# Optimization experiments

Hardware: AMD Instinct MI355X
Metric: run time of the kernel (lower is better)

## Reference

```python
import jax, jax.numpy as jnp
import numpy as np

N_HEADS = 8
D_EMBED = 512
D_HEAD = D_EMBED // N_HEADS  # used only for the scale factor, as in the source


def setup_inputs() -> dict:
    key = jax.random.key(0)
    k1, k2, k3, k4, k5 = jax.random.split(key, 5)
    B, S, D = 4, 4096, D_EMBED
    s = 1.0 / np.sqrt(D)
    return {
        "x": jax.random.normal(k1, (B, S, D), dtype=jnp.float32),
        "w_in": jax.random.normal(k2, (3 * D, D), dtype=jnp.float32) * s,
        "b_in": jax.random.normal(k3, (3 * D,), dtype=jnp.float32) * 0.01,
        "w_out": jax.random.normal(k4, (D, D), dtype=jnp.float32) * s,
        "b_out": jax.random.normal(k5, (D,), dtype=jnp.float32) * 0.01,
    }


def reference(x, w_in, b_in, w_out, b_out):
    # in_proj: torch Linear y = x @ W.T + b ; chunk into q,k,v along last dim
    qkv = jnp.einsum("bsd,ed->bse", x, w_in) + b_in  # [B,S,3D]
    q, k, v = jnp.split(qkv, 3, axis=-1)  # each [B,S,D]
    # NOTE: source never splits into heads; attention over full d_embed,
    # but scaled by sqrt(d_head) = sqrt(d_embed / n_heads).
    scores = jnp.einsum("bqd,bkd->bqk", q, k) / np.sqrt(D_HEAD)  # [B,S,S]
    weight = jax.nn.softmax(scores, axis=-1)
    out = jnp.einsum("bqk,bkd->bqd", weight, v)  # [B,S,D]
    out = jnp.einsum("bsd,ed->bse", out, w_out) + b_out
    return out
```

## Files before the change

### kernel.cpp

```cpp
#include <hip/hip_runtime.h>

typedef __bf16 bf16x8 __attribute__((ext_vector_type(8)));
typedef float f32x4 __attribute__((ext_vector_type(4)));

#define MFMA16(a, b, c) __builtin_amdgcn_mfma_f32_16x16x32_bf16(a, b, c, 0, 0, 0)
#define LOG2E 1.44269504088896340736f

__device__ __forceinline__ unsigned short f2bf(float f) {
  union { float f; unsigned u; } v; v.f = f;
  return (unsigned short)((v.u + 0x7fffu + ((v.u >> 16) & 1u)) >> 16);
}
__device__ __forceinline__ bf16x8 ld_frag(const unsigned short* p) {
  return *(const bf16x8*)p;
}
__device__ __forceinline__ void gld_lds16(const unsigned short* g, unsigned short* l) {
  __builtin_amdgcn_global_load_lds(
      (const __attribute__((address_space(1))) unsigned int*)(const void*)g,
      (__attribute__((address_space(3))) unsigned int*)(void*)l, 16, 0, 0);
}

__global__ void cvt_f2bf(const float* __restrict__ in,
                         unsigned short* __restrict__ out, int n4) {
  int i = blockIdx.x * blockDim.x + threadIdx.x;
  if (i < n4) {
    float4 v = ((const float4*)in)[i];
    ushort4 o;
    o.x = f2bf(v.x); o.y = f2bf(v.y); o.z = f2bf(v.z); o.w = f2bf(v.w);
    ((ushort4*)out)[i] = o;
  }
}

__global__ void gemm_bt(const unsigned short* __restrict__ A,
                        const unsigned short* __restrict__ B,
                        const float* __restrict__ bias,
                        float* __restrict__ outf,
                        unsigned short* __restrict__ qbuf,
                        unsigned short* __restrict__ kbuf,
                        unsigned short* __restrict__ vtbuf,
                        int M, int N, int K, int mode) {
  __shared__ alignas(16) unsigned short As[128 * 32];
  __shared__ alignas(16) unsigned short Bs[128 * 32];
  const int n0 = blockIdx.x * 128, m0 = blockIdx.y * 128;
  const int tid = threadIdx.x;
  const int l = tid & 63, w = tid >> 6;
  const int quad = l >> 4, c = l & 15;
  const int wm = (w >> 1) * 64, wn = (w & 1) * 64;

  f32x4 acc[4][4] = {};
  const int kiters = K >> 5;
  for (int kt = 0; kt < kiters; ++kt) {
    __syncthreads();
    const int kk = kt * 32 + (l & 3) * 8;
    const int row = l >> 2;
#pragma unroll
    for (int i = 0; i < 2; ++i) {
      const int rbase = i * 64 + w * 16;
      gld_lds16(&A[(size_t)(m0 + rbase + row) * K + kk], &As[rbase * 32]);
      gld_lds16(&B[(size_t)(n0 + rbase + row) * K + kk], &Bs[rbase * 32]);
    }
    __syncthreads();
    bf16x8 af[4], bfr[4];
#pragma unroll
    for (int t = 0; t < 4; ++t) {
      af[t] = ld_frag(&As[(wm + t * 16 + c) * 32 + quad * 8]);
      bfr[t] = ld_frag(&Bs[(wn + t * 16 + c) * 32 + quad * 8]);
    }
#pragma unroll
    for (int mt = 0; mt < 4; ++mt)
#pragma unroll
      for (int nt = 0; nt < 4; ++nt)
        acc[mt][nt] = MFMA16(af[mt], bfr[nt], acc[mt][nt]);
  }

#pragma unroll
  for (int nt = 0; nt < 4; ++nt) {
    const int n = n0 + wn + nt * 16 + c;
    const float bsum = bias[n];
#pragma unroll
    for (int mt = 0; mt < 4; ++mt) {
      const int mbase = m0 + wm + mt * 16 + quad * 4;
      if (mode == 0) {
#pragma unroll
        for (int r = 0; r < 4; ++r)
          outf[(size_t)(mbase + r) * N + n] = acc[mt][nt][r] + bsum;
      } else if (n < 1024) {
        unsigned short* dst = (n < 512) ? qbuf : kbuf;
        const int nn = n & 511;
#pragma unroll
        for (int r = 0; r < 4; ++r)
          dst[(size_t)(mbase + r) * 512 + nn] = f2bf(acc[mt][nt][r] + bsum);
      } else {
        const int d = n - 1024;
        const int bb = mbase >> 12, s = mbase & 4095;
        ushort4 pk;
        pk.x = f2bf(acc[mt][nt][0] + bsum);
        pk.y = f2bf(acc[mt][nt][1] + bsum);
        pk.z = f2bf(acc[mt][nt][2] + bsum);
        pk.w = f2bf(acc[mt][nt][3] + bsum);
        *(ushort4*)&vtbuf[((size_t)bb * 512 + d) * 4096 + s] = pk;
      }
    }
  }
}

#define KROW 520
#define PROW 40
#define PBUF (64 * PROW)

__global__ __launch_bounds__(256, 2) void attn_kernel(
    const unsigned short* __restrict__ Q, const unsigned short* __restrict__ Kb,
    const unsigned short* __restrict__ Vt, unsigned short* __restrict__ part0,
    unsigned short* __restrict__ part1, float2* __restrict__ mlbuf) {
  __shared__ alignas(16) unsigned short k_lds[32 * KROW];
  __shared__ alignas(16) unsigned short v_lds[512 * 32];
  __shared__ alignas(16) unsigned short p_lds[2 * PBUF];
  __shared__ float alpha_s[64];
  __shared__ int flag_s[4];

  const int bid = blockIdx.x;
  const int xcd = bid & 7;
  const int b = xcd >> 1;
  const int half = (bid >> 3) & 1;
  const int qt = (bid >> 4) | ((xcd & 1) << 5);
  const int s0 = qt * 64;
  const int kvbase = half * 2048;
  const int tid = threadIdx.x;
  const int l = tid & 63, w = tid >> 6;
  const int quad = l >> 4, c = l & 15;
  const size_t boff = (size_t)b * 4096 * 512;

  const unsigned short* Kbase = Kb + boff;
  const unsigned short* Vbase = Vt + (size_t)b * 512 * 4096;

  auto stage_k = [&](int kv0) {
#pragma unroll
    for (int i = 0; i < 8; ++i) {
      const int row = i * 4 + w;
      gld_lds16(&Kbase[(size_t)(kv0 + row) * 512 + l * 8], &k_lds[row * KROW]);
    }
  };
  auto stage_v = [&](int kv0) {
#pragma unroll
    for (int i = 0; i < 8; ++i) {
      const int dbase = (i * 4 + w) * 16;
      const int d = dbase + (l >> 2);
      const int jl = (l & 3) ^ ((d >> 1) & 3);
      gld_lds16(&Vbase[(size_t)d * 4096 + kv0 + jl * 8], &v_lds[dbase * 32]);
    }
  };

  stage_k(kvbase);
  stage_v(kvbase);

  bf16x8 qf[16];
  {
    const unsigned short* qrow = Q + boff + (size_t)(s0 + w * 16 + c) * 512;
#pragma unroll
    for (int ks = 0; ks < 16; ++ks) qf[ks] = ld_frag(&qrow[ks * 32 + quad * 8]);
  }

  f32x4 o[8][4] = {};
  float m_run = -1e30f, l_run = 0.f;

  const float C1 = 0.125f * LOG2E;

  auto qk_softmax = [&](int i) {
    f32x4 sa[2][2] = {};
    __builtin_amdgcn_s_setprio(1);
#pragma unroll
    for (int ks = 0; ks < 16; ++ks) {
      const unsigned short* kr = &k_lds[c * KROW + ks * 32 + quad * 8];
      bf16x8 kf0 = ld_frag(kr);
      bf16x8 kf1 = ld_frag(kr + 16 * KROW);
      sa[0][ks & 1] = MFMA16(kf0, qf[ks], sa[0][ks & 1]);
      sa[1][ks & 1] = MFMA16(kf1, qf[ks], sa[1][ks & 1]);
    }
    __builtin_amdgcn_s_setprio(0);
    const f32x4 s0v = sa[0][0] + sa[0][1];
    const f32x4 s1v = sa[1][0] + sa[1][1];

    float m8 = fmaxf(fmaxf(fmaxf(s0v[0], s0v[1]), fmaxf(s0v[2], s0v[3])),
                     fmaxf(fmaxf(s1v[0], s1v[1]), fmaxf(s1v[2], s1v[3])));
    m8 = fmaxf(m8, __shfl_xor(m8, 16));
    m8 = fmaxf(m8, __shfl_xor(m8, 32));

    const bool need = __any(m8 - m_run > 8.0f);
    float alpha = 1.0f;
    if (need) {
      const float mn = fmaxf(m_run, m8);
      alpha = exp2f((m_run - mn) * C1);
      m_run = mn;
      l_run *= alpha;
    }

    float p0[4], p1[4], s8 = 0.f;
#pragma unroll
    for (int r = 0; r < 4; ++r) {
      p0[r] = exp2f((s0v[r] - m_run) * C1);
      p1[r] = exp2f((s1v[r] - m_run) * C1);
      s8 += p0[r] + p1[r];
    }
    unsigned short* prow = &p_lds[(i & 1) * PBUF + (w * 16 + c) * PROW];
    ushort4 pk0, pk1;
    pk0.x = f2bf(p0[0]); pk0.y = f2bf(p0[1]); pk0.z = f2bf(p0[2]); pk0.w = f2bf(p0[3]);
    pk1.x = f2bf(p1[0]); pk1.y = f2bf(p1[1]); pk1.z = f2bf(p1[2]); pk1.w = f2bf(p1[3]);
    *(ushort4*)&prow[quad * 4] = pk0;
    *(ushort4*)&prow[16 + quad * 4] = pk1;

    s8 += __shfl_xor(s8, 16);
    s8 += __shfl_xor(s8, 32);
    l_run += s8;

    if (quad == 0) alpha_s[w * 16 + c] = alpha;
    if (l == 0) flag_s[w] = need ? 1 : 0;
  };

  const int jp8 = (quad ^ ((c >> 1) & 3)) * 8;

  asm volatile("s_waitcnt vmcnt(0)" ::: "memory");
  __builtin_amdgcn_sched_barrier(0);
  __builtin_amdgcn_s_barrier();
  __builtin_amdgcn_sched_barrier(0);
  qk_softmax(0);

  for (int it = 0; it < 64; ++it) {
    asm volatile("s_waitcnt vmcnt(0) lgkmcnt(0)" ::: "memory");
    __builtin_amdgcn_sched_barrier(0);
    __builtin_amdgcn_s_barrier();
    __builtin_amdgcn_sched_barrier(0);

    if (it + 1 < 64) stage_k(kvbase + (it + 1) * 32);

    const int f0 = flag_s[0], f1 = flag_s[1], f2 = flag_s[2], f3 = flag_s[3];
    if (f0) {
      const float a = alpha_s[c];
#pragma unroll
      for (int t = 0; t < 8; ++t) o[t][0] *= a;
    }
    if (f1) {
      const float a = alpha_s[16 + c];
#pragma unroll
      for (int t = 0; t < 8; ++t) o[t][1] *= a;
    }
    if (f2) {
      const float a = alpha_s[32 + c];
#pragma unroll
      for (int t = 0; t < 8; ++t) o[t][2] *= a;
    }
    if (f3) {
      const float a = alpha_s[48 + c];
#pragma unroll
      for (int t = 0; t < 8; ++t) o[t][3] *= a;
    }

    const unsigned short* pb = &p_lds[(it & 1) * PBUF];
    const bf16x8 pf0 = ld_frag(&pb[(size_t)c * PROW + quad * 8]);
    const bf16x8 pf1 = ld_frag(&pb[(size_t)(16 + c) * PROW + quad * 8]);
    const bf16x8 pf2 = ld_frag(&pb[(size_t)(32 + c) * PROW + quad * 8]);
    const bf16x8 pf3 = ld_frag(&pb[(size_t)(48 + c) * PROW + quad * 8]);
    __builtin_amdgcn_s_setprio(1);
#pragma unroll
    for (int t = 0; t < 8; ++t) {
      const bf16x8 vf = ld_frag(&v_lds[(w * 128 + t * 16 + c) * 32 + jp8]);
      o[t][0] = MFMA16(vf, pf0, o[t][0]);
      o[t][1] = MFMA16(vf, pf1, o[t][1]);
      o[t][2] = MFMA16(vf, pf2, o[t][2]);
      o[t][3] = MFMA16(vf, pf3, o[t][3]);
    }
    __builtin_amdgcn_s_setprio(0);

    asm volatile("s_waitcnt lgkmcnt(0)" ::: "memory");
    __builtin_amdgcn_sched_barrier(0);
    __builtin_amdgcn_s_barrier();
    __builtin_amdgcn_sched_barrier(0);

    if (it + 1 < 64) {
      stage_v(kvbase + (it + 1) * 32);
      asm volatile("s_waitcnt vmcnt(8)" ::: "memory");
      __builtin_amdgcn_sched_barrier(0);
      __builtin_amdgcn_s_barrier();
      __builtin_amdgcn_sched_barrier(0);
      qk_softmax(it + 1);
    }
  }

  if (quad == 0) {
    alpha_s[w * 16 + c] = l_run;
    float2 ml; ml.x = m_run; ml.y = l_run;
    mlbuf[(size_t)half * 16384 + b * 4096 + s0 + w * 16 + c] = ml;
  }
  __syncthreads();
  const float linv0 = 1.0f / alpha_s[c];
  const float linv1 = 1.0f / alpha_s[16 + c];
  const float linv2 = 1.0f / alpha_s[32 + c];
  const float linv3 = 1.0f / alpha_s[48 + c];

  unsigned short* part = half ? part1 : part0;
  unsigned short* obase = part + boff + (size_t)s0 * 512 + w * 128 + quad * 4;
#pragma unroll
  for (int t = 0; t < 8; ++t) {
    const float li[4] = {linv0, linv1, linv2, linv3};
#pragma unroll
    for (int j = 0; j < 4; ++j) {
      ushort4 pk;
      pk.x = f2bf(o[t][j][0] * li[j]);
      pk.y = f2bf(o[t][j][1] * li[j]);
      pk.z = f2bf(o[t][j][2] * li[j]);
      pk.w = f2bf(o[t][j][3] * li[j]);
      *(ushort4*)&obase[(size_t)(j * 16 + c) * 512 + t * 16] = pk;
    }
  }
}

__global__ void merge_halves(const unsigned short* __restrict__ p1,
                             const float2* __restrict__ mlbuf,
                             unsigned short* __restrict__ p0out) {
  const int i = blockIdx.x * blockDim.x + threadIdx.x;
  const int row = i >> 6;
  const float2 a = mlbuf[row];
  const float2 bb = mlbuf[16384 + row];
  const float C1 = 0.125f * LOG2E;
  const float M = fmaxf(a.x, bb.x);
  float w0 = a.y * exp2f((a.x - M) * C1);
  float w1 = bb.y * exp2f((bb.x - M) * C1);
  const float inv = 1.0f / (w0 + w1);
  w0 *= inv; w1 *= inv;
  bf16x8 v0 = *(const bf16x8*)(p0out + (size_t)i * 8);
  bf16x8 v1 = *(const bf16x8*)(p1 + (size_t)i * 8);
  ushort4 o0, o1;
  o0.x = f2bf(w0 * (float)v0[0] + w1 * (float)v1[0]);
  o0.y = f2bf(w0 * (float)v0[1] + w1 * (float)v1[1]);
  o0.z = f2bf(w0 * (float)v0[2] + w1 * (float)v1[2]);
  o0.w = f2bf(w0 * (float)v0[3] + w1 * (float)v1[3]);
  o1.x = f2bf(w0 * (float)v0[4] + w1 * (float)v1[4]);
  o1.y = f2bf(w0 * (float)v0[5] + w1 * (float)v1[5]);
  o1.z = f2bf(w0 * (float)v0[6] + w1 * (float)v1[6]);
  o1.w = f2bf(w0 * (float)v0[7] + w1 * (float)v1[7]);
  *(ushort4*)(p0out + (size_t)i * 8) = o0;
  *(ushort4*)(p0out + (size_t)i * 8 + 4) = o1;
}

extern "C" void kernel_launch(void* const* d_in, const int* in_sizes, int n_in,
                              void* d_out, int out_size, void* d_ws, size_t ws_size,
                              hipStream_t stream) {
  const float* x = (const float*)d_in[0];
  const float* w_in = (const float*)d_in[1];
  const float* b_in = (const float*)d_in[2];
  const float* w_out = (const float*)d_in[3];
  const float* b_out = (const float*)d_in[4];
  float* out = (float*)d_out;

  const size_t MTOT = (size_t)4 * 4096 * 512;
  unsigned short* q = (unsigned short*)d_ws;
  unsigned short* k = q + MTOT;
  unsigned short* vt = k + MTOT;
  unsigned short* xbf = vt + MTOT;
  unsigned short* part1 = xbf + MTOT;
  unsigned short* w_in_bf = part1 + MTOT;
  unsigned short* w_out_bf = w_in_bf + 1536 * 512;
  float2* mlbuf = (float2*)(w_out_bf + 512 * 512);

  cvt_f2bf<<<dim3((int)(MTOT / 4 / 256)), 256, 0, stream>>>(x, xbf,
                                                            (int)(MTOT / 4));
  cvt_f2bf<<<dim3(768), 256, 0, stream>>>(w_in, w_in_bf, 1536 * 512 / 4);
  cvt_f2bf<<<dim3(256), 256, 0, stream>>>(w_out, w_out_bf, 512 * 512 / 4);

  gemm_bt<<<dim3(12, 128), 256, 0, stream>>>(xbf, w_in_bf, b_in, nullptr, q, k,
                                             vt, 16384, 1536, 512, 1);
  attn_kernel<<<dim3(512), 256, 0, stream>>>(q, k, vt, xbf, part1, mlbuf);
  merge_halves<<<dim3(4096), 256, 0, stream>>>(part1, mlbuf, xbf);
  gemm_bt<<<dim3(4, 128), 256, 0, stream>>>(xbf, w_out_bf, b_out, out, nullptr,
                                            nullptr, nullptr, 16384, 512, 512,
                                            0);
}
```

Baseline: 413.0 us.

## Fuse x fp32-to-bf16 conversion and split-KV merge into GEMM A-tile loads

The QKV projection GEMM now reads fp32 x directly and converts it to bf16 in registers before writing the A tile to LDS. The output projection GEMM performs the two-half softmax merge while loading its A tile. This removes the standalone x conversion kernel, the merge kernel, and their global round trips. A-tile loads are software-prefetched one k-step ahead with manual waitcnt barriers. The cost is extra per-tile ALU work, with the merge and conversion repeated across N-blocks (12x for the QKV conversion, 4x for the merge), plus more register pressure.

Measured after the change: 731.7 us. +77.2%, slower.

```diff
diff --git a/kernel.cpp b/kernel.cpp
--- a/kernel.cpp
+++ b/kernel.cpp
@@ -30,7 +30,8 @@
   }
 }
 
-__global__ void gemm_bt(const unsigned short* __restrict__ A,
+__global__ void gemm_bt(const float* __restrict__ Af,
+                        const unsigned short* __restrict__ A16,
                         const unsigned short* __restrict__ B,
                         const float* __restrict__ bias,
                         float* __restrict__ outf,
@@ -45,20 +46,83 @@
   const int l = tid & 63, w = tid >> 6;
   const int quad = l >> 4, c = l & 15;
   const int wm = (w >> 1) * 64, wn = (w & 1) * 64;
+  const int row = l >> 2;
+  const int col8 = (l & 3) * 8;
+  const float C1m = 0.125f * LOG2E;
+
+  const unsigned short* p1base = qbuf;
+  const float2* ml = (const float2*)kbuf;
+
+  float4 ar[2][2];
+  bf16x8 mr0[2], mr1[2];
+  float2 mla[2], mlb[2];
+
+  auto aload = [&](int kt) {
+    const int kk = kt * 32 + col8;
+#pragma unroll
+    for (int i = 0; i < 2; ++i) {
+      const int r = m0 + i * 64 + w * 16 + row;
+      if (mode == 1) {
+        const float* ap = Af + (size_t)r * K + kk;
+        ar[i][0] = *(const float4*)ap;
+        ar[i][1] = *(const float4*)(ap + 4);
+      } else {
+        mr0[i] = ld_frag(&A16[(size_t)r * K + kk]);
+        mr1[i] = ld_frag(&p1base[(size_t)r * K + kk]);
+        mla[i] = ml[r];
+        mlb[i] = ml[16384 + r];
+      }
+    }
+  };
+  auto awrite = [&]() {
+#pragma unroll
+    for (int i = 0; i < 2; ++i) {
+      union { bf16x8 v; unsigned short s[8]; } pk;
+      if (mode == 1) {
+        pk.s[0] = f2bf(ar[i][0].x); pk.s[1] = f2bf(ar[i][0].y);
+        pk.s[2] = f2bf(ar[i][0].z); pk.s[3] = f2bf(ar[i][0].w);
+        pk.s[4] = f2bf(ar[i][1].x); pk.s[5] = f2bf(ar[i][1].y);
+        pk.s[6] = f2bf(ar[i][1].z); pk.s[7] = f2bf(ar[i][1].w);
+      } else {
+        const float Mx = fmaxf(mla[i].x, mlb[i].x);
+        float w0 = mla[i].y * exp2f((mla[i].x - Mx) * C1m);
+        float w1 = mlb[i].y * exp2f((mlb[i].x - Mx) * C1m);
+        const float inv = 1.0f / (w0 + w1);
+        w0 *= inv; w1 *= inv;
+#pragma unroll
+        for (int e = 0; e < 8; ++e)
+          pk.s[e] = f2bf(w0 * (float)mr0[i][e] + w1 * (float)mr1[i][e]);
+      }
+      *(bf16x8*)&As[(i * 64 + w * 16) * 32 + l * 8] = pk.v;
+    }
+  };
 
   f32x4 acc[4][4] = {};
   const int kiters = K >> 5;
+  aload(0);
   for (int kt = 0; kt < kiters; ++kt) {
     __syncthreads();
-    const int kk = kt * 32 + (l & 3) * 8;
-    const int row = l >> 2;
+    awrite();
+    const int kk = kt * 32 + col8;
 #pragma unroll
     for (int i = 0; i < 2; ++i) {
       const int rbase = i * 64 + w * 16;
-      gld_lds16(&A[(size_t)(m0 + rbase + row) * K + kk], &As[rbase * 32]);
       gld_lds16(&B[(size_t)(n0 + rbase + row) * K + kk], &Bs[rbase * 32]);
     }
-    __syncthreads();
+    if (kt + 1 < kiters) {
+      aload(kt + 1);
+      if (mode == 1) {
+        asm volatile("s_waitcnt vmcnt(4) lgkmcnt(0)" ::: "memory");
+      } else {
+        asm volatile("s_waitcnt vmcnt(8) lgkmcnt(0)" ::: "memory");
+      }
+    } else {
+      asm volatile("s_waitcnt vmcnt(0) lgkmcnt(0)" ::: "memory");
+    }
+    __builtin_amdgcn_sched_barrier(0);
+    __builtin_amdgcn_s_barrier();
+    __builtin_amdgcn_sched_barrier(0);
+
     bf16x8 af[4], bfr[4];
 #pragma unroll
     for (int t = 0; t < 4; ++t) {
@@ -79,16 +143,16 @@
 #pragma unroll
     for (int mt = 0; mt < 4; ++mt) {
       const int mbase = m0 + wm + mt * 16 + quad * 4;
-      if (mode == 0) {
-#pragma unroll
-        for (int r = 0; r < 4; ++r)
-          outf[(size_t)(mbase + r) * N + n] = acc[mt][nt][r] + bsum;
+      if (mode != 1) {
+#pragma unroll
+        for (int r2 = 0; r2 < 4; ++r2)
+          outf[(size_t)(mbase + r2) * N + n] = acc[mt][nt][r2] + bsum;
       } else if (n < 1024) {
         unsigned short* dst = (n < 512) ? qbuf : kbuf;
         const int nn = n & 511;
 #pragma unroll
-        for (int r = 0; r < 4; ++r)
-          dst[(size_t)(mbase + r) * 512 + nn] = f2bf(acc[mt][nt][r] + bsum);
+        for (int r2 = 0; r2 < 4; ++r2)
+          dst[(size_t)(mbase + r2) * 512 + nn] = f2bf(acc[mt][nt][r2] + bsum);
       } else {
         const int d = n - 1024;
         const int bb = mbase >> 12, s = mbase & 4095;
@@ -312,34 +376,6 @@
   }
 }
 
-__global__ void merge_halves(const unsigned short* __restrict__ p1,
-                             const float2* __restrict__ mlbuf,
-                             unsigned short* __restrict__ p0out) {
-  const int i = blockIdx.x * blockDim.x + threadIdx.x;
-  const int row = i >> 6;
-  const float2 a = mlbuf[row];
-  const float2 bb = mlbuf[16384 + row];
-  const float C1 = 0.125f * LOG2E;
-  const float M = fmaxf(a.x, bb.x);
-  float w0 = a.y * exp2f((a.x - M) * C1);
-  float w1 = bb.y * exp2f((bb.x - M) * C1);
-  const float inv = 1.0f / (w0 + w1);
-  w0 *= inv; w1 *= inv;
-  bf16x8 v0 = *(const bf16x8*)(p0out + (size_t)i * 8);
-  bf16x8 v1 = *(const bf16x8*)(p1 + (size_t)i * 8);
-  ushort4 o0, o1;
-  o0.x = f2bf(w0 * (float)v0[0] + w1 * (float)v1[0]);
-  o0.y = f2bf(w0 * (float)v0[1] + w1 * (float)v1[1]);
-  o0.z = f2bf(w0 * (float)v0[2] + w1 * (float)v1[2]);
-  o0.w = f2bf(w0 * (float)v0[3] + w1 * (float)v1[3]);
-  o1.x = f2bf(w0 * (float)v0[4] + w1 * (float)v1[4]);
-  o1.y = f2bf(w0 * (float)v0[5] + w1 * (float)v1[5]);
-  o1.z = f2bf(w0 * (float)v0[6] + w1 * (float)v1[6]);
-  o1.w = f2bf(w0 * (float)v0[7] + w1 * (float)v1[7]);
-  *(ushort4*)(p0out + (size_t)i * 8) = o0;
-  *(ushort4*)(p0out + (size_t)i * 8 + 4) = o1;
-}
-
 extern "C" void kernel_launch(void* const* d_in, const int* in_sizes, int n_in,
                               void* d_out, int out_size, void* d_ws, size_t ws_size,
                               hipStream_t stream) {
@@ -354,22 +390,20 @@
   unsigned short* q = (unsigned short*)d_ws;
   unsigned short* k = q + MTOT;
   unsigned short* vt = k + MTOT;
-  unsigned short* xbf = vt + MTOT;
-  unsigned short* part1 = xbf + MTOT;
+  unsigned short* part0 = vt + MTOT;
+  unsigned short* part1 = part0 + MTOT;
   unsigned short* w_in_bf = part1 + MTOT;
   unsigned short* w_out_bf = w_in_bf + 1536 * 512;
   float2* mlbuf = (float2*)(w_out_bf + 512 * 512);
 
-  cvt_f2bf<<<dim3((int)(MTOT / 4 / 256)), 256, 0, stream>>>(x, xbf,
-                                                            (int)(MTOT / 4));
   cvt_f2bf<<<dim3(768), 256, 0, stream>>>(w_in, w_in_bf, 1536 * 512 / 4);
   cvt_f2bf<<<dim3(256), 256, 0, stream>>>(w_out, w_out_bf, 512 * 512 / 4);
 
-  gemm_bt<<<dim3(12, 128), 256, 0, stream>>>(xbf, w_in_bf, b_in, nullptr, q, k,
-                                             vt, 16384, 1536, 512, 1);
-  attn_kernel<<<dim3(512), 256, 0, stream>>>(q, k, vt, xbf, part1, mlbuf);
-  merge_halves<<<dim3(4096), 256, 0, stream>>>(part1, mlbuf, xbf);
-  gemm_bt<<<dim3(4, 128), 256, 0, stream>>>(xbf, w_out_bf, b_out, out, nullptr,
-                                            nullptr, nullptr, 16384, 512, 512,
-                                            0);
-}
+  gemm_bt<<<dim3(12, 128), 256, 0, stream>>>(x, nullptr, w_in_bf, b_in,
+                                             nullptr, q, k, vt, 16384, 1536,
+                                             512, 1);
+  attn_kernel<<<dim3(512), 256, 0, stream>>>(q, k, vt, part0, part1, mlbuf);
+  gemm_bt<<<dim3(4, 128), 256, 0, stream>>>(nullptr, part0, w_out_bf, b_out,
+                                            out, part1, (unsigned short*)mlbuf,
+                                            nullptr, 16384, 512, 512, 2);
+}
```
